# Optimization experiments

Measured on AMD Instinct MI355X. Metric: run time of the kernel, lower is better.

Reference implementation:

```python
import jax, jax.numpy as jnp
import numpy as np

NEG_SLOPE = 0.2
N_NODES = 50000
N_EDGES = 800000
NUM_GRAPHS = 128
IN_F, HID_F, OUT_F = 64, 64, 64


def _gat_layer(x, src, dst, W, a_src, a_dst, b, n_nodes):
    # x: [N, Fin] -> out: [N, Fout]; single-head PyG GATConv with self-loops
    xp = x @ W                                   # [N, Fout]
    alpha_src = xp @ a_src                       # [N]
    alpha_dst = xp @ a_dst                       # [N]
    e = jax.nn.leaky_relu(alpha_src[src] + alpha_dst[dst], NEG_SLOPE)  # [E]
    # segment softmax over incoming edges of each dst node
    m = jax.ops.segment_max(e, dst, num_segments=n_nodes)
    ex = jnp.exp(e - m[dst])
    denom = jax.ops.segment_sum(ex, dst, num_segments=n_nodes)
    alpha = ex / denom[dst]                      # [E]
    out = jax.ops.segment_sum(alpha[:, None] * xp[src], dst, num_segments=n_nodes)
    return out + b


def setup_inputs() -> dict:
    key = jax.random.key(0)
    ks = jax.random.split(key, 12)
    x = jax.random.normal(ks[0], (N_NODES, IN_F), dtype=jnp.float32)
    edge_index = jax.random.randint(ks[1], (2, N_EDGES), 0, N_NODES, dtype=jnp.int64 if jax.config.jax_enable_x64 else jnp.int32)
    batch = jnp.sort(jax.random.randint(ks[2], (N_NODES,), 0, NUM_GRAPHS, dtype=edge_index.dtype))
    s = 0.1
    W1 = jax.random.normal(ks[3], (IN_F, HID_F), dtype=jnp.float32) * s
    att_src1 = jax.random.normal(ks[4], (HID_F,), dtype=jnp.float32) * s
    att_dst1 = jax.random.normal(ks[5], (HID_F,), dtype=jnp.float32) * s
    b1 = jax.random.normal(ks[6], (HID_F,), dtype=jnp.float32) * s
    W2 = jax.random.normal(ks[7], (HID_F, OUT_F), dtype=jnp.float32) * s
    att_src2 = jax.random.normal(ks[8], (OUT_F,), dtype=jnp.float32) * s
    att_dst2 = jax.random.normal(ks[9], (OUT_F,), dtype=jnp.float32) * s
    b2 = jax.random.normal(ks[10], (OUT_F,), dtype=jnp.float32) * s
    return {"x": x, "edge_index": edge_index, "batch": batch,
            "W1": W1, "att_src1": att_src1, "att_dst1": att_dst1, "b1": b1,
            "W2": W2, "att_src2": att_src2, "att_dst2": att_dst2, "b2": b2}


def reference(x, edge_index, batch, W1, att_src1, att_dst1, b1, W2, att_src2, att_dst2, b2):
    n = x.shape[0]
    # add self-loops (PyG GATConv default)
    loops = jnp.arange(n, dtype=edge_index.dtype)
    src = jnp.concatenate([edge_index[0], loops])
    dst = jnp.concatenate([edge_index[1], loops])
    h = _gat_layer(x, src, dst, W1, att_src1, att_dst1, b1, n)
    h = jax.nn.relu(h)  # dropout = identity at eval
    h = _gat_layer(h, src, dst, W2, att_src2, att_dst2, b2, n)
    h = jax.nn.relu(h)
    # scatter_mean over graphs
    sums = jax.ops.segment_sum(h, batch, num_segments=NUM_GRAPHS)
    counts = jax.ops.segment_sum(jnp.ones((n,), dtype=h.dtype), batch, num_segments=NUM_GRAPHS)
    return sums / jnp.maximum(counts, 1.0)[:, None]
```

## Files before the change

kernel.cpp:

```cpp
#include <hip/hip_runtime.h>
#include <hip/hip_fp16.h>

#define FEAT 64
#define BK   64
#define CAP  1536
#define MAXB 1024
#define SEPT 16
#define CHUNK (256 * SEPT)
#define LG   4
#define SLOT 28
#define MAXC 256

typedef _Float16 f16;
typedef __attribute__((ext_vector_type(8))) _Float16 f16x8;
typedef __attribute__((ext_vector_type(4))) float    f32x4;

struct GemmSm {
    union {
        struct { f16 Xs[64][72]; f16 Wt[64][72]; };
        float Cs[4][16][68];
    };
    float asl[64], adl[64];
};

__device__ __forceinline__ int lower_bound_i(const int* a, int n, int key)
{
    int lo = 0, hi = n;
    while (lo < hi) {
        const int mid = (lo + hi) >> 1;
        if (a[mid] < key) lo = mid + 1; else hi = mid;
    }
    return lo;
}

__device__ __forceinline__ void gemm_tile(
    GemmSm& sm, int row0, const float* __restrict__ xin,
    const float* __restrict__ W, const float* __restrict__ avs,
    const float* __restrict__ avd, unsigned* __restrict__ xph,
    float* __restrict__ as_, float* __restrict__ ad_, int n)
{
    const int t = threadIdx.x;
    const int lane = t & 63;
    const int wave = t >> 6;

    if (t < 64) sm.asl[t] = avs[t];
    else if (t < 128) sm.adl[t - 64] = avd[t - 64];

    for (int i = t; i < 64 * 16; i += 256) {
        const int r = i >> 4, c4 = (i & 15) << 2;
        const int gr = row0 + r;
        float4 v = make_float4(0.f, 0.f, 0.f, 0.f);
        if (gr < n) v = *(const float4*)(xin + (size_t)gr * FEAT + c4);
        sm.Xs[r][c4 + 0] = (f16)v.x; sm.Xs[r][c4 + 1] = (f16)v.y;
        sm.Xs[r][c4 + 2] = (f16)v.z; sm.Xs[r][c4 + 3] = (f16)v.w;
    }
    for (int i = t; i < 64 * 16; i += 256) {
        const int k = i >> 4, c4 = (i & 15) << 2;
        const float4 v = *(const float4*)(W + k * FEAT + c4);
        sm.Wt[c4 + 0][k] = (f16)v.x; sm.Wt[c4 + 1][k] = (f16)v.y;
        sm.Wt[c4 + 2][k] = (f16)v.z; sm.Wt[c4 + 3][k] = (f16)v.w;
    }
    __syncthreads();

    const int mrow = (wave << 4) + (lane & 15);
    const int kg = lane >> 4;
    const f16x8 a0 = *(const f16x8*)(&sm.Xs[mrow][kg * 8]);
    const f16x8 a1 = *(const f16x8*)(&sm.Xs[mrow][32 + kg * 8]);

    f32x4 acc[4];
#pragma unroll
    for (int nt = 0; nt < 4; ++nt) {
        const int ncol = nt * 16 + (lane & 15);
        const f16x8 b0 = *(const f16x8*)(&sm.Wt[ncol][kg * 8]);
        const f16x8 b1 = *(const f16x8*)(&sm.Wt[ncol][32 + kg * 8]);
        f32x4 c = {0.f, 0.f, 0.f, 0.f};
        c = __builtin_amdgcn_mfma_f32_16x16x32_f16(a0, b0, c, 0, 0, 0);
        c = __builtin_amdgcn_mfma_f32_16x16x32_f16(a1, b1, c, 0, 0, 0);
        acc[nt] = c;
    }
    __syncthreads();

#pragma unroll
    for (int nt = 0; nt < 4; ++nt)
#pragma unroll
        for (int reg = 0; reg < 4; ++reg)
            sm.Cs[wave][(lane >> 4) * 4 + reg][nt * 16 + (lane & 15)] = acc[nt][reg];

    for (int i = lane; i < 16 * 32; i += 64) {
        const int r = i >> 5, fp = i & 31;
        const int node = row0 + (wave << 4) + r;
        if (node < n) {
            const __half2 pk = __floats2half2_rn(sm.Cs[wave][r][2 * fp],
                                                 sm.Cs[wave][r][2 * fp + 1]);
            xph[(size_t)node * 32 + fp] = *(const unsigned*)&pk;
        }
    }
    {
        const int r = lane >> 2, q = lane & 3;
        float s1 = 0.f, s2 = 0.f;
#pragma unroll
        for (int j = 0; j < 16; ++j) {
            const int c = q * 16 + j;
            const float v = sm.Cs[wave][r][c];
            s1 += v * sm.asl[c];
            s2 += v * sm.adl[c];
        }
        s1 += __shfl_xor(s1, 1); s1 += __shfl_xor(s1, 2);
        s2 += __shfl_xor(s2, 1); s2 += __shfl_xor(s2, 2);
        const int node = row0 + (wave << 4) + r;
        if (q == 0 && node < n) { as_[node] = s1; ad_[node] = s2; }
    }
}

__global__ __launch_bounds__(256) void scatter_gemm1_kernel(
    const int* __restrict__ src, const int* __restrict__ dst,
    unsigned* __restrict__ ebufS, int* __restrict__ cntG,
    const float* __restrict__ x, const float* __restrict__ W,
    const float* __restrict__ a_src, const float* __restrict__ a_dst,
    unsigned* __restrict__ xph, float* __restrict__ as_, float* __restrict__ ad_,
    const int* __restrict__ batch, float* __restrict__ ginv,
    float* __restrict__ outZ,
    int n, int E, int nbuck, int nchunks, int G)
{
    __shared__ union {
        int hist[MAXB];
        GemmSm g;
    } sm;
    __shared__ int lb[132];

    const int t = threadIdx.x;

    if (blockIdx.x < (unsigned)nchunks) {
        for (int i = t; i < nbuck; i += 256) sm.hist[i] = 0;
        __syncthreads();

        const int e0 = blockIdx.x * CHUNK;
#pragma unroll
        for (int k = 0; k < SEPT; ++k) {
            const int e = e0 + t + k * 256;
            if (e < E) {
                const int s_ = src[e], d = dst[e];
                const int bk = d >> 6;
                const unsigned code = ((unsigned)s_ << 6) | (unsigned)(d & 63);
                const int rk = atomicAdd(&sm.hist[bk], 1);
                if (rk < SLOT)
                    ebufS[((size_t)bk * nchunks + blockIdx.x) * SLOT + rk] = code;
            }
        }
        __syncthreads();
        for (int i = t; i < nbuck; i += 256)
            cntG[(size_t)i * nchunks + blockIdx.x] = min(sm.hist[i], SLOT);
    } else if (blockIdx.x < (unsigned)(nchunks + (n + 63) / 64)) {
        gemm_tile(sm.g, (blockIdx.x - nchunks) * 64, x, W, a_src, a_dst,
                  xph, as_, ad_, n);
    } else {
        if (t <= G) lb[t] = lower_bound_i(batch, n, t);
        __syncthreads();
        if (t < G) ginv[t] = 1.f / fmaxf((float)(lb[t + 1] - lb[t]), 1.f);
        for (int i = t; i < G * FEAT; i += 256) outZ[i] = 0.f;
    }
}

struct PC {
    int node, g, gc, st, en;
    float w0, w1, w2, w3, asg;
    uint4 x0, x1, x2, x3, xg;
};

__device__ __forceinline__ void fma8(float* a, const uint4 xv, const float wv)
{
    const __half2 p0 = *(const __half2*)&xv.x;
    const __half2 p1 = *(const __half2*)&xv.y;
    const __half2 p2 = *(const __half2*)&xv.z;
    const __half2 p3 = *(const __half2*)&xv.w;
    a[0] += wv * __low2float(p0);  a[1] += wv * __high2float(p0);
    a[2] += wv * __low2float(p1);  a[3] += wv * __high2float(p1);
    a[4] += wv * __low2float(p2);  a[5] += wv * __high2float(p2);
    a[6] += wv * __low2float(p3);  a[7] += wv * __high2float(p3);
}

__device__ __forceinline__ void pc_issue(PC& P, int pair, int np, int q, int fo,
    int g0, int n, const int* startsL, const unsigned* scode, const float* sw,
    const float* __restrict__ as_, const uint4* __restrict__ xph4)
{
    P.node = pair * 2 + np;
    P.g  = g0 + P.node;
    P.gc = (P.g < n) ? P.g : (n - 1);
    P.st = startsL[P.node];
    P.en = startsL[P.node + 1];
    const int i0 = P.st + q;
    unsigned c0 = 0, c1 = 0, c2 = 0, c3 = 0;
    P.w0 = 0.f; P.w1 = 0.f; P.w2 = 0.f; P.w3 = 0.f;
    if (i0      < P.en) { c0 = scode[i0];      P.w0 = sw[i0]; }
    if (i0 + 4  < P.en) { c1 = scode[i0 + 4];  P.w1 = sw[i0 + 4]; }
    if (i0 + 8  < P.en) { c2 = scode[i0 + 8];  P.w2 = sw[i0 + 8]; }
    if (i0 + 12 < P.en) { c3 = scode[i0 + 12]; P.w3 = sw[i0 + 12]; }
    P.x0 = xph4[(size_t)(c0 >> 6) * 8 + fo];
    P.x1 = xph4[(size_t)(c1 >> 6) * 8 + fo];
    P.x2 = xph4[(size_t)(c2 >> 6) * 8 + fo];
    P.x3 = xph4[(size_t)(c3 >> 6) * 8 + fo];
    P.xg = xph4[(size_t)P.gc * 8 + fo];
    P.asg = as_[P.gc];
}

__device__ __forceinline__ void pc_consume(const PC& P, int q, int fo,
    const unsigned* scode, const float* sw, const uint4* __restrict__ xph4,
    float* a, float& wsum)
{
    fma8(a, P.x0, P.w0); fma8(a, P.x1, P.w1);
    fma8(a, P.x2, P.w2); fma8(a, P.x3, P.w3);
    wsum += (P.w0 + P.w1) + (P.w2 + P.w3);

    int i = P.st + q + 16;
    for (; i + 12 < P.en; i += 16) {
        const unsigned c0 = scode[i];
        const unsigned c1 = scode[i + 4];
        const unsigned c2 = scode[i + 8];
        const unsigned c3 = scode[i + 12];
        const float w0 = sw[i], w1 = sw[i + 4], w2 = sw[i + 8], w3 = sw[i + 12];
        const uint4 x0 = xph4[(size_t)(c0 >> 6) * 8 + fo];
        const uint4 x1 = xph4[(size_t)(c1 >> 6) * 8 + fo];
        const uint4 x2 = xph4[(size_t)(c2 >> 6) * 8 + fo];
        const uint4 x3 = xph4[(size_t)(c3 >> 6) * 8 + fo];
        fma8(a, x0, w0); fma8(a, x1, w1); fma8(a, x2, w2); fma8(a, x3, w3);
        wsum += (w0 + w1) + (w2 + w3);
    }
    for (; i < P.en; i += 4) {
        const unsigned c0 = scode[i];
        const float w0 = sw[i];
        const uint4 xv = xph4[(size_t)(c0 >> 6) * 8 + fo];
        fma8(a, xv, w0);
        wsum += w0;
    }
}

__device__ __forceinline__ void pc_reduce(float* a, float& wsum)
{
#pragma unroll
    for (int j = 0; j < 8; ++j) {
        a[j] += __shfl_xor(a[j], 8);
        a[j] += __shfl_xor(a[j], 16);
    }
    wsum += __shfl_xor(wsum, 8);
    wsum += __shfl_xor(wsum, 16);
}

__device__ __forceinline__ void pc_epi_h(const PC& P, int q, int fo,
    const float* adb, float* a, float wsum, const float4 bA, const float4 bB,
    float* __restrict__ hout, int hstride, int n)
{
    pc_reduce(a, wsum);
    float tt = P.asg + adb[P.node];
    tt = (tt >= 0.f) ? tt : 0.2f * tt;
    const float wself = __expf(tt);
    const __half2 s0 = *(const __half2*)&P.xg.x;
    const __half2 s1 = *(const __half2*)&P.xg.y;
    const __half2 s2 = *(const __half2*)&P.xg.z;
    const __half2 s3 = *(const __half2*)&P.xg.w;
    const float dinv = 1.f / (wsum + wself);

    if (q == 0 && P.g < n) {
        float4 vA, vB;
        vA.x = fmaxf((a[0] + wself * __low2float(s0))  * dinv + bA.x, 0.f);
        vA.y = fmaxf((a[1] + wself * __high2float(s0)) * dinv + bA.y, 0.f);
        vA.z = fmaxf((a[2] + wself * __low2float(s1))  * dinv + bA.z, 0.f);
        vA.w = fmaxf((a[3] + wself * __high2float(s1)) * dinv + bA.w, 0.f);
        vB.x = fmaxf((a[4] + wself * __low2float(s2))  * dinv + bB.x, 0.f);
        vB.y = fmaxf((a[5] + wself * __high2float(s2)) * dinv + bB.y, 0.f);
        vB.z = fmaxf((a[6] + wself * __low2float(s3))  * dinv + bB.z, 0.f);
        vB.w = fmaxf((a[7] + wself * __high2float(s3)) * dinv + bB.w, 0.f);
        *(float4*)(hout + (size_t)P.node * hstride + 8 * fo)     = vA;
        *(float4*)(hout + (size_t)P.node * hstride + 8 * fo + 4) = vB;
    }
}

__device__ __forceinline__ void pc_epi_pool(const PC& P, int q, int fo,
    int wave, int np, const float* adb, float* a, float wsum,
    const float4 bA, const float4 bB, const int* batchL, int gbase,
    float (*gpartW)[2][LG][FEAT], const float* __restrict__ ginv,
    float* __restrict__ out, int n)
{
    pc_reduce(a, wsum);
    float tt = P.asg + adb[P.node];
    tt = (tt >= 0.f) ? tt : 0.2f * tt;
    const float wself = __expf(tt);
    const __half2 s0 = *(const __half2*)&P.xg.x;
    const __half2 s1 = *(const __half2*)&P.xg.y;
    const __half2 s2 = *(const __half2*)&P.xg.z;
    const __half2 s3 = *(const __half2*)&P.xg.w;
    const float dinv = 1.f / (wsum + wself);

    if (q == 0 && P.g < n) {
        float4 vA, vB;
        vA.x = fmaxf((a[0] + wself * __low2float(s0))  * dinv + bA.x, 0.f);
        vA.y = fmaxf((a[1] + wself * __high2float(s0)) * dinv + bA.y, 0.f);
        vA.z = fmaxf((a[2] + wself * __low2float(s1))  * dinv + bA.z, 0.f);
        vA.w = fmaxf((a[3] + wself * __high2float(s1)) * dinv + bA.w, 0.f);
        vB.x = fmaxf((a[4] + wself * __low2float(s2))  * dinv + bB.x, 0.f);
        vB.y = fmaxf((a[5] + wself * __high2float(s2)) * dinv + bB.y, 0.f);
        vB.z = fmaxf((a[6] + wself * __low2float(s3))  * dinv + bB.z, 0.f);
        vB.w = fmaxf((a[7] + wself * __high2float(s3)) * dinv + bB.w, 0.f);

        const int lg = batchL[P.node] - gbase;
        if (lg < LG) {
            float* p = &gpartW[wave][np][lg][8 * fo];
            float4 oA = *(float4*)p;
            float4 oB = *(float4*)(p + 4);
            oA.x += vA.x; oA.y += vA.y; oA.z += vA.z; oA.w += vA.w;
            oB.x += vB.x; oB.y += vB.y; oB.z += vB.z; oB.w += vB.w;
            *(float4*)p = oA;
            *(float4*)(p + 4) = oB;
        } else {
            const int gg = batchL[P.node];
            const float gi = ginv[gg];
            float* o = out + (size_t)gg * FEAT + 8 * fo;
            atomicAdd(o + 0, vA.x * gi); atomicAdd(o + 1, vA.y * gi);
            atomicAdd(o + 2, vA.z * gi); atomicAdd(o + 3, vA.w * gi);
            atomicAdd(o + 4, vB.x * gi); atomicAdd(o + 5, vB.y * gi);
            atomicAdd(o + 6, vB.z * gi); atomicAdd(o + 7, vB.w * gi);
        }
    }
}

__global__ __launch_bounds__(512) void sortagg1_gemm2_kernel(
    const int* __restrict__ cntG, const unsigned* __restrict__ ebufS,
    unsigned* __restrict__ ebuf2, int* __restrict__ startsG,
    const float* __restrict__ asA, const float* __restrict__ adA,
    const uint4* __restrict__ xphA, const float* __restrict__ b1,
    const float* __restrict__ W2, const float* __restrict__ asrc2,
    const float* __restrict__ adst2,
    unsigned* __restrict__ xphB, float* __restrict__ asB, float* __restrict__ adB,
    int n, int nchunks)
{
    __shared__ union { float htile[64][68]; unsigned raw[CAP]; } hu;
    __shared__ union {
        struct { unsigned scode[CAP]; float sw[CAP]; int hist[BK]; int cur[BK]; } a;
        GemmSm g;
    } sm;
    __shared__ int starts[BK + 1];
    __shared__ float adb[BK];
    __shared__ int cntL[MAXC], ofsL[MAXC + 1];

    const int b = blockIdx.x;
    const int t = threadIdx.x;
    const int lane = t & 63, wave = t >> 6;
    const int g0 = b * BK;
    const int row0 = g0;

    if (t < BK) {
        sm.a.hist[t] = 0;
        adb[t] = (g0 + t < n) ? adA[g0 + t] : 0.f;
    }
    if (t < nchunks) cntL[t] = cntG[(size_t)b * nchunks + t];
    __syncthreads();

    if (wave == 0) {
        int carry = 0;
        for (int c0 = 0; c0 < nchunks; c0 += 64) {
            const int idx = c0 + lane;
            int v = (idx < nchunks) ? cntL[idx] : 0;
            const int orig = v;
#pragma unroll
            for (int o = 1; o < 64; o <<= 1) {
                const int u = __shfl_up(v, o);
                if (lane >= o) v += u;
            }
            if (idx < nchunks) ofsL[idx] = v - orig + carry;
            carry += __shfl(v, 63);
        }
        if (lane == 0) ofsL[nchunks] = carry;
    }
    __syncthreads();
    int cnt = ofsL[nchunks];
    if (cnt > CAP) cnt = CAP;

    {
        const unsigned* region = ebufS + (size_t)b * nchunks * SLOT;
        const int tot = nchunks * SLOT;
        for (int i = t; i < tot; i += 512) {
            const int c = i / SLOT, s = i - c * SLOT;
            if (s < cntL[c]) {
                const int o = ofsL[c] + s;
                if (o < CAP) hu.raw[o] = region[i];
            }
        }
    }
    __syncthreads();

    unsigned c3r[3];
#pragma unroll
    for (int k = 0; k < 3; ++k) {
        const int i = t + k * 512;
        if (i < cnt) { c3r[k] = hu.raw[i]; atomicAdd(&sm.a.hist[c3r[k] & 63], 1); }
    }
    __syncthreads();
    if (wave == 0) {
        int v = sm.a.hist[lane];
#pragma unroll
        for (int o = 1; o < 64; o <<= 1) {
            const int u = __shfl_up(v, o);
            if (lane >= o) v += u;
        }
        starts[lane + 1] = v;
        sm.a.cur[lane] = v - sm.a.hist[lane];
        if (lane == 0) starts[0] = 0;
    }
    __syncthreads();
#pragma unroll
    for (int k = 0; k < 3; ++k) {
        const int i = t + k * 512;
        if (i < cnt) { const int p = atomicAdd(&sm.a.cur[c3r[k] & 63], 1); sm.a.scode[p] = c3r[k]; }
    }
    __syncthreads();

    unsigned cc[3]; float vv[3];
#pragma unroll
    for (int k = 0; k < 3; ++k) {
        const int i = t + k * 512;
        if (i < cnt) {
            cc[k] = sm.a.scode[i];
            ebuf2[(size_t)b * CAP + i] = cc[k];
            vv[k] = asA[cc[k] >> 6];
        }
    }
    if (t <= BK) startsG[b * (BK + 1) + t] = starts[t];
#pragma unroll
    for (int k = 0; k < 3; ++k) {
        const int i = t + k * 512;
        if (i < cnt) {
            float tt = vv[k] + adb[cc[k] & 63];
            tt = (tt >= 0.f) ? tt : 0.2f * tt;
            sm.a.sw[i] = __expf(tt);
        }
    }
    __syncthreads();

    {
        const int np = lane >> 5;
        const int q  = (lane >> 3) & 3;
        const int fo = lane & 7;
        const float4 bA = *(const float4*)(b1 + 8 * fo);
        const float4 bB = *(const float4*)(b1 + 8 * fo + 4);
#pragma unroll
        for (int gsel = 0; gsel < 2; ++gsel) {
            PC A, B;
            pc_issue(A, wave + 8 * gsel,      np, q, fo, g0, n,
                     starts, sm.a.scode, sm.a.sw, asA, xphA);
            pc_issue(B, wave + 8 * gsel + 16, np, q, fo, g0, n,
                     starts, sm.a.scode, sm.a.sw, asA, xphA);
            float aA[8] = {0.f, 0.f, 0.f, 0.f, 0.f, 0.f, 0.f, 0.f};
            float wsA = 0.f;
            pc_consume(A, q, fo, sm.a.scode, sm.a.sw, xphA, aA, wsA);
            pc_epi_h(A, q, fo, adb, aA, wsA, bA, bB, &hu.htile[0][0], 68, n);
            float aB[8] = {0.f, 0.f, 0.f, 0.f, 0.f, 0.f, 0.f, 0.f};
            float wsB = 0.f;
            pc_consume(B, q, fo, sm.a.scode, sm.a.sw, xphA, aB, wsB);
            pc_epi_h(B, q, fo, adb, aB, wsB, bA, bB, &hu.htile[0][0], 68, n);
        }
    }
    __syncthreads();

    if (t < 64) sm.g.asl[t] = asrc2[t];
    else if (t < 128) sm.g.adl[t - 64] = adst2[t - 64];

    for (int i = t; i < 64 * 16; i += 512) {
        const int r = i >> 4, c4 = (i & 15) << 2;
        const float4 v = *(const float4*)(&hu.htile[r][c4]);
        sm.g.Xs[r][c4 + 0] = (f16)v.x; sm.g.Xs[r][c4 + 1] = (f16)v.y;
        sm.g.Xs[r][c4 + 2] = (f16)v.z; sm.g.Xs[r][c4 + 3] = (f16)v.w;
    }
    for (int i = t; i < 64 * 16; i += 512) {
        const int k = i >> 4, c4 = (i & 15) << 2;
        const float4 v = *(const float4*)(W2 + k * FEAT + c4);
        sm.g.Wt[c4 + 0][k] = (f16)v.x; sm.g.Wt[c4 + 1][k] = (f16)v.y;
        sm.g.Wt[c4 + 2][k] = (f16)v.z; sm.g.Wt[c4 + 3][k] = (f16)v.w;
    }
    __syncthreads();

    f32x4 acc[4];
    if (wave < 4) {
        const int mrow = (wave << 4) + (lane & 15);
        const int kg = lane >> 4;
        const f16x8 a0 = *(const f16x8*)(&sm.g.Xs[mrow][kg * 8]);
        const f16x8 a1 = *(const f16x8*)(&sm.g.Xs[mrow][32 + kg * 8]);
#pragma unroll
        for (int nt = 0; nt < 4; ++nt) {
            const int ncol = nt * 16 + (lane & 15);
            const f16x8 b0 = *(const f16x8*)(&sm.g.Wt[ncol][kg * 8]);
            const f16x8 b1v = *(const f16x8*)(&sm.g.Wt[ncol][32 + kg * 8]);
            f32x4 cacc = {0.f, 0.f, 0.f, 0.f};
            cacc = __builtin_amdgcn_mfma_f32_16x16x32_f16(a0, b0, cacc, 0, 0, 0);
            cacc = __builtin_amdgcn_mfma_f32_16x16x32_f16(a1, b1v, cacc, 0, 0, 0);
            acc[nt] = cacc;
        }
    }
    __syncthreads();
    if (wave < 4) {
#pragma unroll
        for (int nt = 0; nt < 4; ++nt)
#pragma unroll
            for (int reg = 0; reg < 4; ++reg)
                sm.g.Cs[wave][(lane >> 4) * 4 + reg][nt * 16 + (lane & 15)] = acc[nt][reg];
    }
    __syncthreads();

    for (int i = t; i < 64 * 32; i += 512) {
        const int r = i >> 5, fp = i & 31;
        const int node = row0 + r;
        if (node < n) {
            const __half2 pk = __floats2half2_rn(sm.g.Cs[r >> 4][r & 15][2 * fp],
                                                 sm.g.Cs[r >> 4][r & 15][2 * fp + 1]);
            xphB[(size_t)node * 32 + fp] = *(const unsigned*)&pk;
        }
    }
    if (t < 256) {
        const int r = t >> 2, q = t & 3;
        float s1 = 0.f, s2 = 0.f;
#pragma unroll
        for (int j = 0; j < 16; ++j) {
            const int cidx = q * 16 + j;
            const float v = sm.g.Cs[r >> 4][r & 15][cidx];
            s1 += v * sm.g.asl[cidx];
            s2 += v * sm.g.adl[cidx];
        }
        s1 += __shfl_xor(s1, 1); s1 += __shfl_xor(s1, 2);
        s2 += __shfl_xor(s2, 1); s2 += __shfl_xor(s2, 2);
        const int node = row0 + r;
        if (q == 0 && node < n) { asB[node] = s1; adB[node] = s2; }
    }
}

__global__ __launch_bounds__(512) void agg2_pool_kernel(
    const unsigned* __restrict__ ebuf2, const int* __restrict__ startsG,
    const float* __restrict__ as_, const float* __restrict__ ad_,
    const uint4* __restrict__ xph4, const float* __restrict__ bias,
    const int* __restrict__ batch, const float* __restrict__ ginv,
    float* __restrict__ out, int n, int G)
{
    __shared__ unsigned scode[CAP];
    __shared__ float    sw[CAP];
    __shared__ int startsL[BK + 1];
    __shared__ float adb[BK];
    __shared__ int batchL[BK];
    __shared__ float gpartW[8][2][LG][FEAT];

    const int b = blockIdx.x;
    const int t = threadIdx.x;
    const int lane = t & 63, wave = t >> 6;
    const int g0 = b * BK;

    if (t < BK) {
        const int g = g0 + t;
        adb[t] = (g < n) ? ad_[g] : 0.f;
        batchL[t] = batch[(g < n) ? g : (n - 1)];
    }
    if (t <= BK) startsL[t] = startsG[b * (BK + 1) + t];
    for (int i = t; i < 8 * 2 * LG * FEAT; i += 512) ((float*)gpartW)[i] = 0.f;
    __syncthreads();

    const int cnt = startsL[BK];
    const unsigned* eb = ebuf2 + (size_t)b * CAP;

    unsigned cc[3]; float vv[3];
#pragma unroll
    for (int k = 0; k < 3; ++k) {
        const int i = t + k * 512;
        if (i < cnt) { cc[k] = eb[i]; vv[k] = as_[cc[k] >> 6]; }
    }
#pragma unroll
    for (int k = 0; k < 3; ++k) {
        const int i = t + k * 512;
        if (i < cnt) {
            float tt = vv[k] + adb[cc[k] & 63];
            tt = (tt >= 0.f) ? tt : 0.2f * tt;
            scode[i] = cc[k]; sw[i] = __expf(tt);
        }
    }
    __syncthreads();

    {
        const int np = lane >> 5;
        const int q  = (lane >> 3) & 3;
        const int fo = lane & 7;
        const int gbase = batchL[0];
        const float4 bA = *(const float4*)(bias + 8 * fo);
        const float4 bB = *(const float4*)(bias + 8 * fo + 4);
#pragma unroll
        for (int gsel = 0; gsel < 2; ++gsel) {
            PC A, B;
            pc_issue(A, wave + 8 * gsel,      np, q, fo, g0, n,
                     startsL, scode, sw, as_, xph4);
            pc_issue(B, wave + 8 * gsel + 16, np, q, fo, g0, n,
                     startsL, scode, sw, as_, xph4);
            float aA[8] = {0.f, 0.f, 0.f, 0.f, 0.f, 0.f, 0.f, 0.f};
            float wsA = 0.f;
            pc_consume(A, q, fo, scode, sw, xph4, aA, wsA);
            pc_epi_pool(A, q, fo, wave, np, adb, aA, wsA, bA, bB,
                        batchL, gbase, gpartW, ginv, out, n);
            float aB[8] = {0.f, 0.f, 0.f, 0.f, 0.f, 0.f, 0.f, 0.f};
            float wsB = 0.f;
            pc_consume(B, q, fo, scode, sw, xph4, aB, wsB);
            pc_epi_pool(B, q, fo, wave, np, adb, aB, wsB, bA, bB,
                        batchL, gbase, gpartW, ginv, out, n);
        }
    }
    __syncthreads();

    if (t < LG * FEAT) {
        const int lg = t >> 6, f = t & 63;
        float s = 0.f;
#pragma unroll
        for (int w = 0; w < 8; ++w)
            s += gpartW[w][0][lg][f] + gpartW[w][1][lg][f];
        const int gg = batchL[0] + lg;
        if (s != 0.f && gg < G)
            atomicAdd(&out[(size_t)gg * FEAT + f], s * ginv[gg]);
    }
}

extern "C" void kernel_launch(void* const* d_in, const int* in_sizes, int n_in,
                              void* d_out, int out_size, void* d_ws, size_t ws_size,
                              hipStream_t stream)
{
    const float* x      = (const float*)d_in[0];
    const int*   ei     = (const int*)d_in[1];
    const int*   batch  = (const int*)d_in[2];
    const float* W1     = (const float*)d_in[3];
    const float* asrc1  = (const float*)d_in[4];
    const float* adst1  = (const float*)d_in[5];
    const float* b1     = (const float*)d_in[6];
    const float* W2     = (const float*)d_in[7];
    const float* asrc2  = (const float*)d_in[8];
    const float* adst2  = (const float*)d_in[9];
    const float* b2     = (const float*)d_in[10];

    const int N = in_sizes[2];
    const int E = in_sizes[1] / 2;
    const int G = out_size / FEAT;

    const int* src = ei;
    const int* dst = ei + E;

    const int nbuck   = (N + BK - 1) / BK;
    const int nchunks = (E + CHUNK - 1) / CHUNK;
    const int gemmBlocks = (N + 63) / 64;

    unsigned* xphA    = (unsigned*)d_ws;
    unsigned* xphB    = xphA + (size_t)N * 32;
    float*    asA     = (float*)(xphB + (size_t)N * 32);
    float*    adA     = asA + N;
    float*    asB     = adA + N;
    float*    adB     = asB + N;
    float*    ginv    = adB + N;
    unsigned* ebufS   = (unsigned*)(ginv + G);
    int*      cntG    = (int*)(ebufS + (size_t)nbuck * nchunks * SLOT);
    unsigned* ebuf2   = (unsigned*)(cntG + (size_t)nbuck * nchunks);
    int*      startsG = (int*)(ebuf2 + (size_t)nbuck * CAP);

    scatter_gemm1_kernel<<<nchunks + gemmBlocks + 1, 256, 0, stream>>>(
        src, dst, ebufS, cntG, x, W1, asrc1, adst1, xphA, asA, adA,
        batch, ginv, (float*)d_out, N, E, nbuck, nchunks, G);
    sortagg1_gemm2_kernel<<<nbuck, 512, 0, stream>>>(
        cntG, ebufS, ebuf2, startsG, asA, adA, (const uint4*)xphA, b1,
        W2, asrc2, adst2, xphB, asB, adB, N, nchunks);
    agg2_pool_kernel<<<nbuck, 512, 0, stream>>>(
        ebuf2, startsG, asB, adB, (const uint4*)xphB, b2,
        batch, ginv, (float*)d_out, N, G);
}
```

Before: 166.6 us.

## Enlarge edge chunks, per-wave histograms in sort, split layer-2 GEMM over all waves

Each bucketing block now processes 64 edges per thread, giving fewer chunks (at most 64), more slots per bucket-chunk and a single-pass prefix scan. The local counting sort uses one histogram per wave to cut LDS atomic contention. The second-layer GEMM now runs on all 8 waves, each handling half the columns, instead of 4 waves doing all of them. Larger chunks reduce parallelism in the scatter phase and use more ebufS space per slot. Fixing SLOT at 48 also raises the risk of overflow truncation if a bucket-chunk receives more edges than that.

```diff
diff --git a/kernel.cpp b/kernel.cpp
--- a/kernel.cpp
+++ b/kernel.cpp
@@ -5,11 +5,11 @@
 #define BK   64
 #define CAP  1536
 #define MAXB 1024
-#define SEPT 16
+#define SEPT 64
 #define CHUNK (256 * SEPT)
 #define LG   4
-#define SLOT 28
-#define MAXC 256
+#define SLOT 48
+#define MAXC 64
 
 typedef _Float16 f16;
 typedef __attribute__((ext_vector_type(8))) _Float16 f16x8;
@@ -135,7 +135,6 @@
         __syncthreads();
 
         const int e0 = blockIdx.x * CHUNK;
-#pragma unroll
         for (int k = 0; k < SEPT; ++k) {
             const int e = e0 + t + k * 256;
             if (e < E) {
@@ -334,7 +333,10 @@
 {
     __shared__ union { float htile[64][68]; unsigned raw[CAP]; } hu;
     __shared__ union {
-        struct { unsigned scode[CAP]; float sw[CAP]; int hist[BK]; int cur[BK]; } a;
+        struct {
+            unsigned scode[CAP]; float sw[CAP];
+            int hist8[8][64]; int cur8[8][64];
+        } a;
         GemmSm g;
     } sm;
     __shared__ int starts[BK + 1];
@@ -347,28 +349,21 @@
     const int g0 = b * BK;
     const int row0 = g0;
 
-    if (t < BK) {
-        sm.a.hist[t] = 0;
-        adb[t] = (g0 + t < n) ? adA[g0 + t] : 0.f;
-    }
+    sm.a.hist8[wave][lane] = 0;
+    if (t < BK) adb[t] = (g0 + t < n) ? adA[g0 + t] : 0.f;
     if (t < nchunks) cntL[t] = cntG[(size_t)b * nchunks + t];
     __syncthreads();
 
     if (wave == 0) {
-        int carry = 0;
-        for (int c0 = 0; c0 < nchunks; c0 += 64) {
-            const int idx = c0 + lane;
-            int v = (idx < nchunks) ? cntL[idx] : 0;
-            const int orig = v;
-#pragma unroll
-            for (int o = 1; o < 64; o <<= 1) {
-                const int u = __shfl_up(v, o);
-                if (lane >= o) v += u;
-            }
-            if (idx < nchunks) ofsL[idx] = v - orig + carry;
-            carry += __shfl(v, 63);
-        }
-        if (lane == 0) ofsL[nchunks] = carry;
+        int v = (lane < nchunks) ? cntL[lane] : 0;
+        const int orig = v;
+#pragma unroll
+        for (int o = 1; o < 64; o <<= 1) {
+            const int u = __shfl_up(v, o);
+            if (lane >= o) v += u;
+        }
+        if (lane < nchunks) ofsL[lane] = v - orig;
+        if (lane == 63) ofsL[nchunks] = v;
     }
     __syncthreads();
     int cnt = ofsL[nchunks];
@@ -391,25 +386,35 @@
 #pragma unroll
     for (int k = 0; k < 3; ++k) {
         const int i = t + k * 512;
-        if (i < cnt) { c3r[k] = hu.raw[i]; atomicAdd(&sm.a.hist[c3r[k] & 63], 1); }
+        if (i < cnt) { c3r[k] = hu.raw[i]; atomicAdd(&sm.a.hist8[wave][c3r[k] & 63], 1); }
     }
     __syncthreads();
     if (wave == 0) {
-        int v = sm.a.hist[lane];
+        int tot = 0;
+#pragma unroll
+        for (int w = 0; w < 8; ++w) {
+            sm.a.cur8[w][lane] = tot;
+            tot += sm.a.hist8[w][lane];
+        }
+        int v = tot;
 #pragma unroll
         for (int o = 1; o < 64; o <<= 1) {
             const int u = __shfl_up(v, o);
             if (lane >= o) v += u;
         }
         starts[lane + 1] = v;
-        sm.a.cur[lane] = v - sm.a.hist[lane];
         if (lane == 0) starts[0] = 0;
     }
+    __syncthreads();
+    sm.a.cur8[wave][lane] += starts[lane];
     __syncthreads();
 #pragma unroll
     for (int k = 0; k < 3; ++k) {
         const int i = t + k * 512;
-        if (i < cnt) { const int p = atomicAdd(&sm.a.cur[c3r[k] & 63], 1); sm.a.scode[p] = c3r[k]; }
+        if (i < cnt) {
+            const int p = atomicAdd(&sm.a.cur8[wave][c3r[k] & 63], 1);
+            sm.a.scode[p] = c3r[k];
+        }
     }
     __syncthreads();
 
@@ -477,15 +482,17 @@
     }
     __syncthreads();
 
-    f32x4 acc[4];
-    if (wave < 4) {
-        const int mrow = (wave << 4) + (lane & 15);
+    {
+        const int rowgrp  = wave & 3;
+        const int colhalf = wave >> 2;
+        const int mrow = (rowgrp << 4) + (lane & 15);
         const int kg = lane >> 4;
         const f16x8 a0 = *(const f16x8*)(&sm.g.Xs[mrow][kg * 8]);
         const f16x8 a1 = *(const f16x8*)(&sm.g.Xs[mrow][32 + kg * 8]);
-#pragma unroll
-        for (int nt = 0; nt < 4; ++nt) {
-            const int ncol = nt * 16 + (lane & 15);
+        f32x4 acc[2];
+#pragma unroll
+        for (int nt = 0; nt < 2; ++nt) {
+            const int ncol = colhalf * 32 + nt * 16 + (lane & 15);
             const f16x8 b0 = *(const f16x8*)(&sm.g.Wt[ncol][kg * 8]);
             const f16x8 b1v = *(const f16x8*)(&sm.g.Wt[ncol][32 + kg * 8]);
             f32x4 cacc = {0.f, 0.f, 0.f, 0.f};
@@ -493,14 +500,13 @@
             cacc = __builtin_amdgcn_mfma_f32_16x16x32_f16(a1, b1v, cacc, 0, 0, 0);
             acc[nt] = cacc;
         }
-    }
-    __syncthreads();
-    if (wave < 4) {
-#pragma unroll
-        for (int nt = 0; nt < 4; ++nt)
+        __syncthreads();
+#pragma unroll
+        for (int nt = 0; nt < 2; ++nt)
 #pragma unroll
             for (int reg = 0; reg < 4; ++reg)
-                sm.g.Cs[wave][(lane >> 4) * 4 + reg][nt * 16 + (lane & 15)] = acc[nt][reg];
+                sm.g.Cs[rowgrp][(lane >> 4) * 4 + reg]
+                        [colhalf * 32 + nt * 16 + (lane & 15)] = acc[nt][reg];
     }
     __syncthreads();
 
```

New measurement: 187.0 us. 12.3% more time.
